# Performance work log

Hardware: AMD Instinct MI355X
Metric: run time of the kernel (lower is better)

The kernel has to match this reference:

```python
import jax, jax.numpy as jnp
import numpy as np

D_MODEL = 1024
NUM_HEADS = 16
HEAD_DIM = D_MODEL // NUM_HEADS


def setup_inputs() -> dict:
    key = jax.random.key(0)
    ks = jax.random.split(key, 10)
    B, L = 2, 2048
    s = 1.0 / np.sqrt(D_MODEL)
    x = jax.random.normal(ks[0], (B, L, D_MODEL), dtype=jnp.float32)
    Wq = jax.random.normal(ks[1], (D_MODEL, D_MODEL), dtype=jnp.float32) * s
    bq = jnp.zeros((D_MODEL,), dtype=jnp.float32)
    Wk = jax.random.normal(ks[2], (D_MODEL, D_MODEL), dtype=jnp.float32) * s
    bk = jnp.zeros((D_MODEL,), dtype=jnp.float32)
    Wv = jax.random.normal(ks[3], (D_MODEL, D_MODEL), dtype=jnp.float32) * s
    bv = jnp.zeros((D_MODEL,), dtype=jnp.float32)
    Wo = jax.random.normal(ks[4], (D_MODEL, D_MODEL), dtype=jnp.float32) * s
    bo = jnp.zeros((D_MODEL,), dtype=jnp.float32)
    # per-head retention decay; torch init is ones, use values near 1 for nontrivial decay
    gamma = jax.random.uniform(ks[5], (NUM_HEADS,), dtype=jnp.float32, minval=0.95, maxval=1.0)
    return {"x": x, "Wq": Wq, "bq": bq, "Wk": Wk, "bk": bk,
            "Wv": Wv, "bv": bv, "Wo": Wo, "bo": bo, "gamma": gamma}


def reference(x, Wq, bq, Wk, bk, Wv, bv, Wo, bo, gamma):
    B, L, D = x.shape
    H, hd = NUM_HEADS, HEAD_DIM
    # projections (torch Linear: x @ W.T + b), split heads -> [B, H, L, hd]
    q = (x @ Wq.T + bq).reshape(B, L, H, hd).transpose(0, 2, 1, 3)
    k = (x @ Wk.T + bk).reshape(B, L, H, hd).transpose(0, 2, 1, 3)
    v = (x @ Wv.T + bv).reshape(B, L, H, hd).transpose(0, 2, 1, 3)
    # per-head decay gamma_h^i applied along the query index (matches torch broadcast)
    idx = jnp.arange(L, dtype=x.dtype)
    decay = gamma[None, :, None, None] ** idx[None, None, :, None]  # [1, H, L, 1]
    scores = jnp.einsum('bhqd,bhkd->bhqk', q, k)  # [B, H, L, L]
    causal = jnp.tril(jnp.ones((L, L), dtype=x.dtype))
    scores = scores * causal[None, None] * decay
    out = jnp.einsum('bhqk,bhkd->bhqd', scores, v)  # [B, H, L, hd]
    out = out.transpose(0, 2, 1, 3).reshape(B, L, D)
    return out @ Wo.T + bo
```

## Files before the change

kernel.cpp:

```cpp
#include <hip/hip_runtime.h>
#include <hip/hip_bf16.h>

#define D_MODEL 1024
#define NUM_HEADS 16
#define HEAD_DIM 64
#define BATCH 2
#define SEQ 2048
#define M_TOT (BATCH*SEQ)
#define CHUNK 64
#define NCHUNK (SEQ/CHUNK)
#define LT 68

typedef __attribute__((ext_vector_type(8))) short bf16x8;
typedef __attribute__((ext_vector_type(8))) unsigned short us16x8;
typedef __attribute__((ext_vector_type(4))) float f32x4;

__device__ inline ushort f2bf(float f) {
    __hip_bfloat16 h = __float2bfloat16(f);
    return __builtin_bit_cast(ushort, h);
}

__device__ inline bf16x8 ld_frag(const ushort* p) {
    struct S { uint2 a, b; };
    S s;
    s.a = *(const uint2*)p;
    s.b = *(const uint2*)(p + 4);
    return __builtin_bit_cast(bf16x8, s);
}

__device__ inline void st16(ushort* dst, uint4 a, uint4 b) {
    *(uint2*)(dst + 0)  = make_uint2(a.x, a.y);
    *(uint2*)(dst + 4)  = make_uint2(a.z, a.w);
    *(uint2*)(dst + 8)  = make_uint2(b.x, b.y);
    *(uint2*)(dst + 12) = make_uint2(b.z, b.w);
}

__device__ inline void load_lds16(const ushort* g, ushort* l) {
    __builtin_amdgcn_global_load_lds(
        (const __attribute__((address_space(1))) unsigned int*)g,
        (__attribute__((address_space(3))) unsigned int*)l, 16, 0, 0);
}

#define XN (M_TOT * D_MODEL)
#define WN (D_MODEL * D_MODEL)
__global__ __launch_bounds__(256) void cast_all_kernel(const float* __restrict__ x,
                                                       const float* __restrict__ Wq,
                                                       const float* __restrict__ Wk,
                                                       const float* __restrict__ Wv,
                                                       const float* __restrict__ Wo,
                                                       ushort* __restrict__ dst) {
    size_t o = ((size_t)blockIdx.x * 256 + threadIdx.x) * 4;
    const float* src;
    if (o < XN)               src = x  + o;
    else if (o < XN + WN)     src = Wq + (o - XN);
    else if (o < XN + 2 * WN) src = Wk + (o - XN - WN);
    else if (o < XN + 3 * WN) src = Wv + (o - XN - 2 * (size_t)WN);
    else                      src = Wo + (o - XN - 3 * (size_t)WN);
    float4 f = *(const float4*)src;
    ushort4 u;
    u.x = f2bf(f.x); u.y = f2bf(f.y); u.z = f2bf(f.z); u.w = f2bf(f.w);
    *(ushort4*)(dst + o) = u;
}

__global__ __launch_bounds__(256) void decay_kernel(const float* __restrict__ gamma,
                                                    float* __restrict__ decay) {
    int idx = blockIdx.x * blockDim.x + threadIdx.x;
    if (idx < SEQ * NUM_HEADS) {
        int i = idx >> 4, h = idx & 15;
        decay[idx] = powf(gamma[h], (float)i);
    }
}

template <int NBUF, int OUT_BF16>
__global__ __launch_bounds__(256) void gemm128(const ushort* __restrict__ A,
                                               const ushort* __restrict__ Bt,
                                               const float* __restrict__ b0,
                                               const float* __restrict__ b1,
                                               const float* __restrict__ b2,
                                               void* __restrict__ o0,
                                               void* __restrict__ o1,
                                               void* __restrict__ o2,
                                               const float* __restrict__ decay) {
    const int K = 1024;
    __shared__ ushort lds_a[128 * 64];
    __shared__ ushort lds_b[128 * 64];
    int t = threadIdx.x;
    int lane = t & 63, w = t >> 6;
    int bm = blockIdx.y * 128, bn = blockIdx.x * 128;
    int wm = (w >> 1) * 64, wn = (w & 1) * 64;

    int lr = lane >> 3, lc = lane & 7;
    int gcol = lc ^ (lr & 7);
    const ushort* aBase = A  + (size_t)(bm + w * 32 + lr) * K + gcol * 8;
    const ushort* bBase = Bt + (size_t)(bn + w * 32 + lr) * K + gcol * 8;
    ushort* aLds = &lds_a[(w * 32) * 64];
    ushort* bLds = &lds_b[(w * 32) * 64];

    f32x4 acc[4][4];
    #pragma unroll
    for (int i = 0; i < 4; i++)
        #pragma unroll
        for (int j = 0; j < 4; j++)
            acc[i][j] = (f32x4){0.f, 0.f, 0.f, 0.f};

    int mrel = lane & 15, kq = lane >> 4;

    for (int k0 = 0; k0 < K; k0 += 64) {
        #pragma unroll
        for (int q = 0; q < 4; q++) {
            load_lds16(aBase + (size_t)q * 8 * K + k0, aLds + q * 512);
            load_lds16(bBase + (size_t)q * 8 * K + k0, bLds + q * 512);
        }
        __syncthreads();
        #pragma unroll
        for (int s = 0; s < 2; s++) {
            bf16x8 af[4], bfv[4];
            #pragma unroll
            for (int i = 0; i < 4; i++) {
                int row = wm + i * 16 + mrel;
                af[i] = ld_frag(&lds_a[row * 64 + (((s * 4 + kq) ^ (row & 7)) * 8)]);
            }
            #pragma unroll
            for (int j = 0; j < 4; j++) {
                int row = wn + j * 16 + mrel;
                bfv[j] = ld_frag(&lds_b[row * 64 + (((s * 4 + kq) ^ (row & 7)) * 8)]);
            }
            #pragma unroll
            for (int i = 0; i < 4; i++)
                #pragma unroll
                for (int j = 0; j < 4; j++)
                    acc[i][j] = __builtin_amdgcn_mfma_f32_16x16x32_bf16(af[i], bfv[j], acc[i][j], 0, 0, 0);
        }
        __syncthreads();
    }

    int quad = lane >> 4;
    int buf = (NBUF == 3) ? (bn >> 10) : 0;
    const float* bias = (buf == 0) ? b0 : (buf == 1) ? b1 : b2;
    void* dstv = (buf == 0) ? o0 : (buf == 1) ? o1 : o2;
    int cbase = ((NBUF == 3) ? (bn & 1023) : bn) + wn;
    #pragma unroll
    for (int j = 0; j < 4; j++) {
        int cl = cbase + j * 16 + mrel;
        float bv = bias[cl];
        #pragma unroll
        for (int i = 0; i < 4; i++) {
            #pragma unroll
            for (int reg = 0; reg < 4; reg++) {
                int row = bm + wm + i * 16 + quad * 4 + reg;
                float v = acc[i][j][reg] + bv;
                if (NBUF == 3 && buf == 0)
                    v *= decay[(row & (SEQ - 1)) * 16 + (cl >> 6)];
                if (OUT_BF16)
                    ((ushort*)dstv)[(size_t)row * 1024 + cl] = f2bf(v);
                else
                    ((float*)dstv)[(size_t)row * 1024 + cl] = v;
            }
        }
    }
}

__global__ __launch_bounds__(256) void chunk_kv_mfma(const ushort* __restrict__ kp,
                                                     const ushort* __restrict__ vp,
                                                     float* __restrict__ states) {
    __shared__ ushort Kt[64 * LT];
    __shared__ ushort Vt[64 * LT];
    int bx = blockIdx.x;
    int c = bx & 31, h = (bx >> 5) & 15, b = bx >> 9;
    int t = threadIdx.x, lane = t & 63, w = t >> 6;
    size_t rowbase = (size_t)(b * SEQ + c * 64);
    int r = t >> 2, cc = t & 3;
    const uint4* gk = (const uint4*)(kp + (rowbase + r) * D_MODEL + h * 64 + cc * 16);
    const uint4* gv = (const uint4*)(vp + (rowbase + r) * D_MODEL + h * 64 + cc * 16);
    uint4 k0 = gk[0], k1 = gk[1], v0 = gv[0], v1 = gv[1];
    {
        us16x8 ka = __builtin_bit_cast(us16x8, k0), kb = __builtin_bit_cast(us16x8, k1);
        us16x8 va = __builtin_bit_cast(us16x8, v0), vb = __builtin_bit_cast(us16x8, v1);
        #pragma unroll
        for (int i = 0; i < 8; i++) {
            Kt[(cc * 16 + i) * LT + r]     = ka[i];
            Kt[(cc * 16 + 8 + i) * LT + r] = kb[i];
            Vt[(cc * 16 + i) * LT + r]     = va[i];
            Vt[(cc * 16 + 8 + i) * LT + r] = vb[i];
        }
    }
    __syncthreads();
    int mrel = lane & 15, q8 = (lane >> 4) * 8, band = w * 16;
    bf16x8 af[2];
    af[0] = ld_frag(&Vt[(band + mrel) * LT + q8]);
    af[1] = ld_frag(&Vt[(band + mrel) * LT + 32 + q8]);
    f32x4 acc[4];
    #pragma unroll
    for (int dt = 0; dt < 4; dt++) acc[dt] = (f32x4){0.f, 0.f, 0.f, 0.f};
    #pragma unroll
    for (int dt = 0; dt < 4; dt++)
        #pragma unroll
        for (int kk = 0; kk < 2; kk++)
            acc[dt] = __builtin_amdgcn_mfma_f32_16x16x32_bf16(
                af[kk], ld_frag(&Kt[(dt * 16 + mrel) * LT + kk * 32 + q8]), acc[dt], 0, 0, 0);
    int quad = lane >> 4;
    float* sp = states + (size_t)bx * 4096;
    #pragma unroll
    for (int dt = 0; dt < 4; dt++)
        #pragma unroll
        for (int reg = 0; reg < 4; reg++)
            sp[(band + quad * 4 + reg) * 64 + dt * 16 + mrel] = acc[dt][reg];
}

__global__ __launch_bounds__(256) void prefix_kernel(const float* __restrict__ states,
                                                     ushort* __restrict__ statesb) {
    int bh = blockIdx.y;
    int e = blockIdx.x * 256 + threadIdx.x;
    const float* src = states + (size_t)bh * NCHUNK * 4096 + e;
    ushort* dst = statesb + (size_t)bh * NCHUNK * 4096 + e;
    float run = 0.f;
    for (int cb = 0; cb < NCHUNK; cb += 8) {
        float vals[8];
        #pragma unroll
        for (int u = 0; u < 8; u++) vals[u] = src[(size_t)(cb + u) * 4096];
        #pragma unroll
        for (int u = 0; u < 8; u++) {
            dst[(size_t)(cb + u) * 4096] = f2bf(run);
            run += vals[u];
        }
    }
}

__global__ __launch_bounds__(256) void attn_mfma(const ushort* __restrict__ qp,
                                                 const ushort* __restrict__ kp,
                                                 const ushort* __restrict__ vp,
                                                 const ushort* __restrict__ statesb,
                                                 ushort* __restrict__ attn_out) {
    __shared__ ushort Qs[64 * LT];
    __shared__ ushort Ks[64 * LT];
    __shared__ ushort Vt[64 * LT];
    __shared__ ushort St[64 * LT];
    __shared__ ushort Ps[64 * LT];
    int bx = blockIdx.x;
    int c = bx & 31, h = (bx >> 5) & 15, b = bx >> 9;
    int t = threadIdx.x, lane = t & 63, w = t >> 6;
    size_t rowbase = (size_t)(b * SEQ + c * 64);
    int r = t >> 2, cc = t & 3;
    {
        const uint4* gq = (const uint4*)(qp + (rowbase + r) * D_MODEL + h * 64 + cc * 16);
        const uint4* gk = (const uint4*)(kp + (rowbase + r) * D_MODEL + h * 64 + cc * 16);
        const uint4* gv = (const uint4*)(vp + (rowbase + r) * D_MODEL + h * 64 + cc * 16);
        const uint4* gs = (const uint4*)(statesb + (size_t)bx * 4096 + t * 16);
        uint4 q0 = gq[0], q1 = gq[1];
        uint4 k0 = gk[0], k1 = gk[1];
        uint4 v0 = gv[0], v1 = gv[1];
        uint4 s0 = gs[0], s1 = gs[1];
        st16(&Qs[r * LT + cc * 16], q0, q1);
        st16(&Ks[r * LT + cc * 16], k0, k1);
        st16(&St[r * LT + cc * 16], s0, s1);
        us16x8 va = __builtin_bit_cast(us16x8, v0), vb = __builtin_bit_cast(us16x8, v1);
        #pragma unroll
        for (int i = 0; i < 8; i++) {
            Vt[(cc * 16 + i) * LT + r]     = va[i];
            Vt[(cc * 16 + 8 + i) * LT + r] = vb[i];
        }
    }
    __syncthreads();

    int mrel = lane & 15, q8 = (lane >> 4) * 8, quad = lane >> 4, band = w * 16;
    bf16x8 af[2];
    af[0] = ld_frag(&Qs[(band + mrel) * LT + q8]);
    af[1] = ld_frag(&Qs[(band + mrel) * LT + 32 + q8]);

    f32x4 oacc[4];
    #pragma unroll
    for (int dt = 0; dt < 4; dt++) oacc[dt] = (f32x4){0.f, 0.f, 0.f, 0.f};
    #pragma unroll
    for (int dt = 0; dt < 4; dt++)
        #pragma unroll
        for (int kk = 0; kk < 2; kk++)
            oacc[dt] = __builtin_amdgcn_mfma_f32_16x16x32_bf16(
                af[kk], ld_frag(&St[(dt * 16 + mrel) * LT + kk * 32 + q8]), oacc[dt], 0, 0, 0);

    f32x4 pacc[4];
    #pragma unroll
    for (int jt = 0; jt < 4; jt++) pacc[jt] = (f32x4){0.f, 0.f, 0.f, 0.f};
    #pragma unroll
    for (int jt = 0; jt < 4; jt++) {
        if (jt <= w) {
            #pragma unroll
            for (int kk = 0; kk < 2; kk++)
                pacc[jt] = __builtin_amdgcn_mfma_f32_16x16x32_bf16(
                    af[kk], ld_frag(&Ks[(jt * 16 + mrel) * LT + kk * 32 + q8]), pacc[jt], 0, 0, 0);
        }
    }
    #pragma unroll
    for (int jt = 0; jt < 4; jt++) {
        #pragma unroll
        for (int reg = 0; reg < 4; reg++) {
            int i = band + quad * 4 + reg;
            int j = jt * 16 + mrel;
            float val = (jt <= w && j <= i) ? pacc[jt][reg] : 0.f;
            Ps[i * LT + j] = f2bf(val);
        }
    }
    __syncthreads();

    bf16x8 pf0 = ld_frag(&Ps[(band + mrel) * LT + q8]);
    #pragma unroll
    for (int dt = 0; dt < 4; dt++)
        oacc[dt] = __builtin_amdgcn_mfma_f32_16x16x32_bf16(
            pf0, ld_frag(&Vt[(dt * 16 + mrel) * LT + q8]), oacc[dt], 0, 0, 0);
    if (w >= 2) {
        bf16x8 pf1 = ld_frag(&Ps[(band + mrel) * LT + 32 + q8]);
        #pragma unroll
        for (int dt = 0; dt < 4; dt++)
            oacc[dt] = __builtin_amdgcn_mfma_f32_16x16x32_bf16(
                pf1, ld_frag(&Vt[(dt * 16 + mrel) * LT + 32 + q8]), oacc[dt], 0, 0, 0);
    }

    #pragma unroll
    for (int dt = 0; dt < 4; dt++) {
        #pragma unroll
        for (int reg = 0; reg < 4; reg++) {
            size_t row = rowbase + band + quad * 4 + reg;
            int col = h * 64 + dt * 16 + mrel;
            attn_out[row * D_MODEL + col] = f2bf(oacc[dt][reg]);
        }
    }
}

extern "C" void kernel_launch(void* const* d_in, const int* in_sizes, int n_in,
                              void* d_out, int out_size, void* d_ws, size_t ws_size,
                              hipStream_t stream) {
    (void)in_sizes; (void)n_in; (void)out_size; (void)ws_size;
    const float* x  = (const float*)d_in[0];
    const float* Wq = (const float*)d_in[1];
    const float* bq = (const float*)d_in[2];
    const float* Wk = (const float*)d_in[3];
    const float* bk = (const float*)d_in[4];
    const float* Wv = (const float*)d_in[5];
    const float* bv = (const float*)d_in[6];
    const float* Wo = (const float*)d_in[7];
    const float* bo = (const float*)d_in[8];
    const float* gamma = (const float*)d_in[9];
    float* out = (float*)d_out;

    uint8_t* w = (uint8_t*)d_ws;
    ushort* xb    = (ushort*)w; w += (size_t)XN * 2;
    ushort* wqkvb = (ushort*)w; w += (size_t)3 * WN * 2;
    ushort* wob   = (ushort*)w; w += (size_t)WN * 2;
    ushort* qb  = (ushort*)w; w += (size_t)XN * 2;
    ushort* kb  = (ushort*)w; w += (size_t)XN * 2;
    ushort* vb  = (ushort*)w; w += (size_t)XN * 2;
    float*  states  = (float*)w;  w += (size_t)BATCH * NUM_HEADS * NCHUNK * 4096 * 4;
    ushort* statesb = (ushort*)w; w += (size_t)BATCH * NUM_HEADS * NCHUNK * 4096 * 2;
    float*  decay   = (float*)w;  w += (size_t)SEQ * NUM_HEADS * 4;

    cast_all_kernel<<<(XN + 4 * WN) / 4 / 256, 256, 0, stream>>>(x, Wq, Wk, Wv, Wo, xb);
    decay_kernel<<<(SEQ * NUM_HEADS) / 256, 256, 0, stream>>>(gamma, decay);

    gemm128<3, 1><<<dim3(3072 / 128, M_TOT / 128), 256, 0, stream>>>(
        xb, wqkvb, bq, bk, bv, qb, kb, vb, decay);

    int nblk = BATCH * NUM_HEADS * NCHUNK;
    chunk_kv_mfma<<<nblk, 256, 0, stream>>>(kb, vb, states);
    prefix_kernel<<<dim3(16, 32), 256, 0, stream>>>(states, statesb);
    attn_mfma<<<nblk, 256, 0, stream>>>(qb, kb, vb, statesb, xb);

    gemm128<1, 0><<<dim3(1024 / 128, M_TOT / 128), 256, 0, stream>>>(
        xb, wob, bo, nullptr, nullptr, out, nullptr, nullptr, nullptr);
}
```

Before: 190.6 us.

## Fuse chunk state, prefix scan and attention into one cooperative kernel

Folds the decay computation into the cast kernel as extra blocks, and replaces three attention-stage launches (chunk KV states, prefix scan, chunk attention) with one cooperative kernel that uses grid-wide syncs between the phases. The chunk states are now stored in bf16 and scanned in place, which drops the fp32 state buffer and two launch gaps. The cost is two grid.sync barriers over 1024 blocks, which need all blocks co-resident, and the prefix scan runs on only half the blocks while the others idle. If the cooperative launch fails, the code falls back to the old three-kernel path.

```diff
diff --git a/kernel.cpp b/kernel.cpp
--- a/kernel.cpp
+++ b/kernel.cpp
@@ -1,5 +1,8 @@
 #include <hip/hip_runtime.h>
 #include <hip/hip_bf16.h>
+#include <hip/hip_cooperative_groups.h>
+
+namespace cg = cooperative_groups;
 
 #define D_MODEL 1024
 #define NUM_HEADS 16
@@ -19,6 +22,10 @@
     __hip_bfloat16 h = __float2bfloat16(f);
     return __builtin_bit_cast(ushort, h);
 }
+__device__ inline float bf2f(ushort u) {
+    unsigned int v = ((unsigned int)u) << 16;
+    return __builtin_bit_cast(float, v);
+}
 
 __device__ inline bf16x8 ld_frag(const ushort* p) {
     struct S { uint2 a, b; };
@@ -43,13 +50,23 @@
 
 #define XN (M_TOT * D_MODEL)
 #define WN (D_MODEL * D_MODEL)
+#define CAST_BLOCKS ((XN + 4 * WN) / 4 / 256)
 __global__ __launch_bounds__(256) void cast_all_kernel(const float* __restrict__ x,
                                                        const float* __restrict__ Wq,
                                                        const float* __restrict__ Wk,
                                                        const float* __restrict__ Wv,
                                                        const float* __restrict__ Wo,
-                                                       ushort* __restrict__ dst) {
-    size_t o = ((size_t)blockIdx.x * 256 + threadIdx.x) * 4;
+                                                       ushort* __restrict__ dst,
+                                                       const float* __restrict__ gamma,
+                                                       float* __restrict__ decay) {
+    int bx = blockIdx.x;
+    if (bx >= CAST_BLOCKS) {
+        int idx = (bx - CAST_BLOCKS) * 256 + threadIdx.x;
+        int i = idx >> 4, h = idx & 15;
+        decay[idx] = powf(gamma[h], (float)i);
+        return;
+    }
+    size_t o = ((size_t)bx * 256 + threadIdx.x) * 4;
     const float* src;
     if (o < XN)               src = x  + o;
     else if (o < XN + WN)     src = Wq + (o - XN);
@@ -60,15 +77,6 @@
     ushort4 u;
     u.x = f2bf(f.x); u.y = f2bf(f.y); u.z = f2bf(f.z); u.w = f2bf(f.w);
     *(ushort4*)(dst + o) = u;
-}
-
-__global__ __launch_bounds__(256) void decay_kernel(const float* __restrict__ gamma,
-                                                    float* __restrict__ decay) {
-    int idx = blockIdx.x * blockDim.x + threadIdx.x;
-    if (idx < SEQ * NUM_HEADS) {
-        int i = idx >> 4, h = idx & 15;
-        decay[idx] = powf(gamma[h], (float)i);
-    }
 }
 
 template <int NBUF, int OUT_BF16>
@@ -160,6 +168,156 @@
     }
 }
 
+__global__ __launch_bounds__(256, 4) void fused_attn(const ushort* __restrict__ qp,
+                                                     const ushort* __restrict__ kp,
+                                                     const ushort* __restrict__ vp,
+                                                     ushort* __restrict__ statesb,
+                                                     ushort* __restrict__ attn_out) {
+    __shared__ ushort B1[64 * LT];
+    __shared__ ushort B2[64 * LT];
+    __shared__ ushort B3[64 * LT];
+    __shared__ ushort B4[64 * LT];
+    cg::grid_group grid = cg::this_grid();
+
+    int bx = blockIdx.x;
+    int c = bx & 31, h = (bx >> 5) & 15, b = bx >> 9;
+    int t = threadIdx.x, lane = t & 63, w = t >> 6;
+    size_t rowbase = (size_t)(b * SEQ + c * 64);
+    int r = t >> 2, cc = t & 3;
+    int mrel = lane & 15, q8 = (lane >> 4) * 8, quad = lane >> 4, band = w * 16;
+
+    {
+        const uint4* gk = (const uint4*)(kp + (rowbase + r) * D_MODEL + h * 64 + cc * 16);
+        const uint4* gv = (const uint4*)(vp + (rowbase + r) * D_MODEL + h * 64 + cc * 16);
+        uint4 k0 = gk[0], k1 = gk[1], v0 = gv[0], v1 = gv[1];
+        st16(&B3[r * LT + cc * 16], k0, k1);
+        us16x8 ka = __builtin_bit_cast(us16x8, k0), kb = __builtin_bit_cast(us16x8, k1);
+        us16x8 va = __builtin_bit_cast(us16x8, v0), vb = __builtin_bit_cast(us16x8, v1);
+        #pragma unroll
+        for (int i = 0; i < 8; i++) {
+            B1[(cc * 16 + i) * LT + r]     = ka[i];
+            B1[(cc * 16 + 8 + i) * LT + r] = kb[i];
+            B2[(cc * 16 + i) * LT + r]     = va[i];
+            B2[(cc * 16 + 8 + i) * LT + r] = vb[i];
+        }
+    }
+    __syncthreads();
+    {
+        bf16x8 af0 = ld_frag(&B2[(band + mrel) * LT + q8]);
+        bf16x8 af1 = ld_frag(&B2[(band + mrel) * LT + 32 + q8]);
+        f32x4 acc[4];
+        #pragma unroll
+        for (int dt = 0; dt < 4; dt++) acc[dt] = (f32x4){0.f, 0.f, 0.f, 0.f};
+        #pragma unroll
+        for (int dt = 0; dt < 4; dt++) {
+            acc[dt] = __builtin_amdgcn_mfma_f32_16x16x32_bf16(
+                af0, ld_frag(&B1[(dt * 16 + mrel) * LT + q8]), acc[dt], 0, 0, 0);
+            acc[dt] = __builtin_amdgcn_mfma_f32_16x16x32_bf16(
+                af1, ld_frag(&B1[(dt * 16 + mrel) * LT + 32 + q8]), acc[dt], 0, 0, 0);
+        }
+        #pragma unroll
+        for (int dt = 0; dt < 4; dt++)
+            #pragma unroll
+            for (int reg = 0; reg < 4; reg++)
+                B4[(band + quad * 4 + reg) * LT + dt * 16 + mrel] = f2bf(acc[dt][reg]);
+    }
+    __syncthreads();
+    {
+        bf16x8 s0 = ld_frag(&B4[r * LT + cc * 16]);
+        bf16x8 s1 = ld_frag(&B4[r * LT + cc * 16 + 8]);
+        uint4* dst = (uint4*)(statesb + (size_t)bx * 4096 + r * 64 + cc * 16);
+        dst[0] = __builtin_bit_cast(uint4, s0);
+        dst[1] = __builtin_bit_cast(uint4, s1);
+    }
+    grid.sync();
+
+    if (c < 16) {
+        ushort* p = statesb + (size_t)(bx >> 5) * NCHUNK * 4096 + c * 256 + t;
+        float run = 0.f;
+        for (int cb = 0; cb < NCHUNK; cb += 8) {
+            float vals[8];
+            #pragma unroll
+            for (int u = 0; u < 8; u++) vals[u] = bf2f(p[(size_t)(cb + u) * 4096]);
+            #pragma unroll
+            for (int u = 0; u < 8; u++) {
+                p[(size_t)(cb + u) * 4096] = f2bf(run);
+                run += vals[u];
+            }
+        }
+    }
+    grid.sync();
+
+    {
+        const uint4* gq = (const uint4*)(qp + (rowbase + r) * D_MODEL + h * 64 + cc * 16);
+        const uint4* gs = (const uint4*)(statesb + (size_t)bx * 4096 + t * 16);
+        uint4 q0 = gq[0], q1 = gq[1];
+        uint4 s0 = gs[0], s1 = gs[1];
+        st16(&B1[r * LT + cc * 16], q0, q1);
+        st16(&B4[(t >> 2) * LT + (t & 3) * 16], s0, s1);
+    }
+    __syncthreads();
+
+    bf16x8 af0 = ld_frag(&B1[(band + mrel) * LT + q8]);
+    bf16x8 af1 = ld_frag(&B1[(band + mrel) * LT + 32 + q8]);
+
+    f32x4 oacc[4];
+    #pragma unroll
+    for (int dt = 0; dt < 4; dt++) oacc[dt] = (f32x4){0.f, 0.f, 0.f, 0.f};
+    #pragma unroll
+    for (int dt = 0; dt < 4; dt++) {
+        oacc[dt] = __builtin_amdgcn_mfma_f32_16x16x32_bf16(
+            af0, ld_frag(&B4[(dt * 16 + mrel) * LT + q8]), oacc[dt], 0, 0, 0);
+        oacc[dt] = __builtin_amdgcn_mfma_f32_16x16x32_bf16(
+            af1, ld_frag(&B4[(dt * 16 + mrel) * LT + 32 + q8]), oacc[dt], 0, 0, 0);
+    }
+
+    f32x4 pacc[4];
+    #pragma unroll
+    for (int jt = 0; jt < 4; jt++) pacc[jt] = (f32x4){0.f, 0.f, 0.f, 0.f};
+    #pragma unroll
+    for (int jt = 0; jt < 4; jt++) {
+        if (jt <= w) {
+            pacc[jt] = __builtin_amdgcn_mfma_f32_16x16x32_bf16(
+                af0, ld_frag(&B3[(jt * 16 + mrel) * LT + q8]), pacc[jt], 0, 0, 0);
+            pacc[jt] = __builtin_amdgcn_mfma_f32_16x16x32_bf16(
+                af1, ld_frag(&B3[(jt * 16 + mrel) * LT + 32 + q8]), pacc[jt], 0, 0, 0);
+        }
+    }
+    #pragma unroll
+    for (int jt = 0; jt < 4; jt++) {
+        #pragma unroll
+        for (int reg = 0; reg < 4; reg++) {
+            int i = band + quad * 4 + reg;
+            int j = jt * 16 + mrel;
+            float val = (jt <= w && j <= i) ? pacc[jt][reg] : 0.f;
+            B1[i * LT + j] = f2bf(val);
+        }
+    }
+
+    bf16x8 pf0 = ld_frag(&B1[(band + mrel) * LT + q8]);
+    #pragma unroll
+    for (int dt = 0; dt < 4; dt++)
+        oacc[dt] = __builtin_amdgcn_mfma_f32_16x16x32_bf16(
+            pf0, ld_frag(&B2[(dt * 16 + mrel) * LT + q8]), oacc[dt], 0, 0, 0);
+    if (w >= 2) {
+        bf16x8 pf1 = ld_frag(&B1[(band + mrel) * LT + 32 + q8]);
+        #pragma unroll
+        for (int dt = 0; dt < 4; dt++)
+            oacc[dt] = __builtin_amdgcn_mfma_f32_16x16x32_bf16(
+                pf1, ld_frag(&B2[(dt * 16 + mrel) * LT + 32 + q8]), oacc[dt], 0, 0, 0);
+    }
+
+    #pragma unroll
+    for (int dt = 0; dt < 4; dt++) {
+        #pragma unroll
+        for (int reg = 0; reg < 4; reg++) {
+            size_t row = rowbase + band + quad * 4 + reg;
+            int col = h * 64 + dt * 16 + mrel;
+            attn_out[row * D_MODEL + col] = f2bf(oacc[dt][reg]);
+        }
+    }
+}
+
 __global__ __launch_bounds__(256) void chunk_kv_mfma(const ushort* __restrict__ kp,
                                                      const ushort* __restrict__ vp,
                                                      float* __restrict__ states) {
@@ -352,16 +510,25 @@
     ushort* statesb = (ushort*)w; w += (size_t)BATCH * NUM_HEADS * NCHUNK * 4096 * 2;
     float*  decay   = (float*)w;  w += (size_t)SEQ * NUM_HEADS * 4;
 
-    cast_all_kernel<<<(XN + 4 * WN) / 4 / 256, 256, 0, stream>>>(x, Wq, Wk, Wv, Wo, xb);
-    decay_kernel<<<(SEQ * NUM_HEADS) / 256, 256, 0, stream>>>(gamma, decay);
+    cast_all_kernel<<<CAST_BLOCKS + (SEQ * NUM_HEADS) / 256, 256, 0, stream>>>(
+        x, Wq, Wk, Wv, Wo, xb, gamma, decay);
 
     gemm128<3, 1><<<dim3(3072 / 128, M_TOT / 128), 256, 0, stream>>>(
         xb, wqkvb, bq, bk, bv, qb, kb, vb, decay);
 
     int nblk = BATCH * NUM_HEADS * NCHUNK;
-    chunk_kv_mfma<<<nblk, 256, 0, stream>>>(kb, vb, states);
-    prefix_kernel<<<dim3(16, 32), 256, 0, stream>>>(states, statesb);
-    attn_mfma<<<nblk, 256, 0, stream>>>(qb, kb, vb, statesb, xb);
+    {
+        const ushort* a0 = qb; const ushort* a1 = kb; const ushort* a2 = vb;
+        ushort* a3 = statesb; ushort* a4 = xb;
+        void* args[] = {&a0, &a1, &a2, &a3, &a4};
+        hipError_t rc = hipLaunchCooperativeKernel((void*)fused_attn, dim3(nblk), dim3(256),
+                                                   args, 0, stream);
+        if (rc != hipSuccess) {
+            chunk_kv_mfma<<<nblk, 256, 0, stream>>>(kb, vb, states);
+            prefix_kernel<<<dim3(16, 32), 256, 0, stream>>>(states, statesb);
+            attn_mfma<<<nblk, 256, 0, stream>>>(qb, kb, vb, statesb, xb);
+        }
+    }
 
     gemm128<1, 0><<<dim3(1024 / 128, M_TOT / 128), 256, 0, stream>>>(
         xb, wob, bo, nullptr, nullptr, out, nullptr, nullptr, nullptr);
```

After: 451.0 us. 137% more time.
